# Kernel tuning notes

Hardware: AMD Instinct MI355X
Metric: run time of the kernel (lower is better)

Reference implementation:

```python
import jax, jax.numpy as jnp
import numpy as np

B, H, L, N = 128, 1024, 256, 64  # batch, d_model, seq len (l_max), SSM state size


def setup_inputs() -> dict:
    key = jax.random.key(0)
    ks = jax.random.split(key, 8)
    x = jax.random.normal(ks[0], (B, H, L), dtype=jnp.float32)
    # S4D init: dt log-uniform in [1e-3, 1e-1], A = -1/2 + i*pi*n, C ~ N(0,1)
    log_dt = jnp.log(10.0 ** jax.random.uniform(ks[1], (H,), minval=-3.0, maxval=-1.0)).astype(jnp.float32)
    A_real_log = jnp.log(0.5 * jnp.ones((H, N), dtype=jnp.float32))
    A_imag = jnp.tile(jnp.pi * jnp.arange(N, dtype=jnp.float32), (H, 1))
    C_re = jax.random.normal(ks[2], (H, N), dtype=jnp.float32)
    C_im = jax.random.normal(ks[3], (H, N), dtype=jnp.float32)
    D = jax.random.normal(ks[4], (H,), dtype=jnp.float32)
    W_out = (jax.random.normal(ks[5], (2 * H, H), dtype=jnp.float32) / np.sqrt(H)).astype(jnp.float32)
    b_out = jnp.zeros((2 * H,), dtype=jnp.float32)
    return dict(x=x, log_dt=log_dt, A_real_log=A_real_log, A_imag=A_imag,
                C_re=C_re, C_im=C_im, D=D, W_out=W_out, b_out=b_out)


def _s4d_kernel(log_dt, A_real_log, A_imag, C_re, C_im, length):
    """S4D convolution kernel (ZOH discretization), shape (H, length)."""
    dt = jnp.exp(log_dt)[:, None]                      # (H, 1)
    A = -jnp.exp(A_real_log) + 1j * A_imag             # (H, N) complex
    C = C_re + 1j * C_im                               # (H, N)
    dtA = A * dt                                       # (H, N)
    C_disc = C * (jnp.exp(dtA) - 1.0) / A              # ZOH-discretized C
    t = jnp.arange(length, dtype=jnp.float32)
    K = jnp.exp(dtA[:, :, None] * t)                   # (H, N, L) Vandermonde
    return 2.0 * jnp.einsum('hn,hnl->hl', C_disc, K).real


def reference(x, log_dt, A_real_log, A_imag, C_re, C_im, D, W_out, b_out):
    Bq, Hq, Lq = x.shape
    k = _s4d_kernel(log_dt, A_real_log, A_imag, C_re, C_im, Lq)  # (H, L)
    n_fft = 2 * Lq
    k_f = jnp.fft.rfft(k, n=n_fft)                     # (H, L+1)
    x_f = jnp.fft.rfft(x, n=n_fft, axis=-1)            # (B, H, L+1)
    y = jnp.fft.irfft(x_f * k_f[None], n=n_fft, axis=-1)[..., :Lq]
    y = y + D[None, :, None] * x                       # skip connection
    y = jax.nn.gelu(y)                                 # FFTConv activation
    # output linear (d_model -> 2*d_model) + GLU over channel dim
    y = jnp.einsum('bhl,gh->bgl', y, W_out) + b_out[None, :, None]
    a, b = jnp.split(y, 2, axis=1)
    return a * jax.nn.sigmoid(b)                       # (B, H, L)
```

## Files before the change

kernel.cpp:

```cpp
#include <hip/hip_runtime.h>
#include <hip/hip_bf16.h>
#include <cstdint>
#include <cstddef>

typedef __bf16 bf16x8 __attribute__((ext_vector_type(8)));
typedef float  f32x4  __attribute__((ext_vector_type(4)));
typedef unsigned short u16x8 __attribute__((ext_vector_type(8)));

__device__ __forceinline__ unsigned short f2bf(float f) {
    unsigned u = __builtin_bit_cast(unsigned, f);
    u += 0x7fffu + ((u >> 16) & 1u);
    return (unsigned short)(u >> 16);
}
__device__ __forceinline__ float bf2f(unsigned short u) {
    unsigned v = ((unsigned)u) << 16;
    return __builtin_bit_cast(float, v);
}
__device__ __forceinline__ float gelu_tanh(float x) {
    float z = 0.7978845608028654f * (x + 0.044715f * x * x * x);
    float e = __expf(2.0f * z);
    float t = 1.0f - 2.0f / (e + 1.0f);
    return 0.5f * x * (1.0f + t);
}

__global__ void k_build(const float* __restrict__ log_dt,
                        const float* __restrict__ arl,
                        const float* __restrict__ aim,
                        const float* __restrict__ cre,
                        const float* __restrict__ cim,
                        const float* __restrict__ Dp,
                        unsigned short* __restrict__ Tg) {
    __shared__ float sRe[64], sIm[64], sCr[64], sCi[64];
    __shared__ float kk[256];
    const int h = blockIdx.x;
    const int t = threadIdx.x;
    if (t < 64) {
        float dt  = expf(log_dt[h]);
        float ar  = -expf(arl[h * 64 + t]);
        float ai  = aim[h * 64 + t];
        float dre = ar * dt, dim = ai * dt;
        float er  = expf(dre);
        float s, c;
        sincosf(dim, &s, &c);
        float em1r = er * c - 1.0f, em1i = er * s;
        float cr = cre[h * 64 + t], ci = cim[h * 64 + t];
        float pr = cr * em1r - ci * em1i;
        float pi = cr * em1i + ci * em1r;
        float inv = 1.0f / (ar * ar + ai * ai);
        sCr[t] = (pr * ar + pi * ai) * inv;
        sCi[t] = (pi * ar - pr * ai) * inv;
        sRe[t] = dre; sIm[t] = dim;
    }
    __syncthreads();
    float acc = 0.0f;
    const float tf = (float)t;
    #pragma unroll 8
    for (int n = 0; n < 64; n++) {
        float er = expf(sRe[n] * tf);
        float s, c;
        sincosf(sIm[n] * tf, &s, &c);
        acc += sCr[n] * er * c - sCi[n] * er * s;
    }
    kk[t] = 2.0f * acc;
    __syncthreads();
    const float Dh = Dp[h];
    unsigned short* dst = Tg + (size_t)h * 16384;
    for (int c = t; c < 1024; c += 256) {
        const int d = c >> 6, q4 = (c >> 4) & 3, mm = c & 15;
        u16x8 hv, lv;
        #pragma unroll
        for (int e = 0; e < 8; e++) {
            const int idx = 16 * d + mm - (q4 * 8 + e);
            float v = (idx >= 0) ? kk[idx] : 0.0f;
            if (idx == 0) v += Dh;
            unsigned short hb = f2bf(v);
            hv[e] = hb;
            lv[e] = f2bf(v - bf2f(hb));
        }
        *(u16x8*)(dst + c * 8)        = hv;
        *(u16x8*)(dst + 8192 + c * 8) = lv;
    }
}

__global__ __launch_bounds__(256, 2)
void conv_mfma(const float* __restrict__ x,
               const unsigned short* __restrict__ Tg,
               unsigned short* __restrict__ yt2) {
    __shared__ __align__(16) unsigned short smem[32768];
    const int h = blockIdx.x, tid = threadIdx.x;
    const int w = tid >> 6, lane = tid & 63, m = lane & 15, q4 = lane >> 4;

    {
        const unsigned short* tg = Tg + (size_t)h * 16384;
        #pragma unroll
        for (int i = 0; i < 8; i++) {
            int q = i * 256 + tid;
            __builtin_amdgcn_global_load_lds(
                (const __attribute__((address_space(1))) void*)(tg + q * 8),
                (__attribute__((address_space(3))) void*)(smem + q * 8), 16, 0, 0);
        }
    }

    const int sb = tid >> 1;
    const float* xrow = x + (((size_t)(sb * 1024 + h)) << 8) + (tid & 1) * 16;

    {
        float4 v0 = *(const float4*)(xrow + 0);
        float4 v1 = *(const float4*)(xrow + 4);
        float4 v2 = *(const float4*)(xrow + 8);
        float4 v3 = *(const float4*)(xrow + 12);
        unsigned short* Xn = smem + 16384;
        const int qb = (tid & 1) * 2;
        #pragma unroll
        for (int s = 0; s < 4; s++) {
            float4 v = (s == 0) ? v0 : (s == 1) ? v1 : (s == 2) ? v2 : v3;
            const int q = qb + (s >> 1), off = (s & 1) * 4;
            ushort4 hv, lv;
            hv.x = f2bf(v.x); lv.x = f2bf(v.x - bf2f(hv.x));
            hv.y = f2bf(v.y); lv.y = f2bf(v.y - bf2f(hv.y));
            hv.z = f2bf(v.z); lv.z = f2bf(v.z - bf2f(hv.z));
            hv.w = f2bf(v.w); lv.w = f2bf(v.w - bf2f(hv.w));
            *(ushort4*)(Xn + (q * 128 + sb) * 8 + off)        = hv;
            *(ushort4*)(Xn + 4096 + (q * 128 + sb) * 8 + off) = lv;
        }
    }

    f32x4 acc[8][4];
    #pragma unroll
    for (int a = 0; a < 8; a++)
        #pragma unroll
        for (int b = 0; b < 4; b++) acc[a][b] = (f32x4){0.f, 0.f, 0.f, 0.f};

    __syncthreads();

    const int fi = (q4 * 16 + m) * 8;

    #pragma unroll 1
    for (int jt = 0; jt < 8; jt++) {
        const unsigned short* Xb = smem + 16384 + (jt & 1) * 8192;
        float4 p0, p1, p2, p3;
        if (jt < 7) {
            const float* xp = xrow + (jt + 1) * 32;
            p0 = *(const float4*)(xp + 0);
            p1 = *(const float4*)(xp + 4);
            p2 = *(const float4*)(xp + 8);
            p3 = *(const float4*)(xp + 12);
        }
        const int j2 = jt << 1;
        const bool a0 = (w      >= j2);
        const bool a1 = (w + 4  >= j2);
        const bool a2 = (w + 8  >= j2);
        const bool a3 = (w + 12 >= j2);
        bf16x8 th0, tl0, th1, tl1, th2, tl2, th3, tl3;
        if (a0) { int d = w      - j2; th0 = *(const bf16x8*)(smem + d * 512 + fi); tl0 = *(const bf16x8*)(smem + 8192 + d * 512 + fi); }
        if (a1) { int d = w + 4  - j2; th1 = *(const bf16x8*)(smem + d * 512 + fi); tl1 = *(const bf16x8*)(smem + 8192 + d * 512 + fi); }
        if (a2) { int d = w + 8  - j2; th2 = *(const bf16x8*)(smem + d * 512 + fi); tl2 = *(const bf16x8*)(smem + 8192 + d * 512 + fi); }
        if (a3) { int d = w + 12 - j2; th3 = *(const bf16x8*)(smem + d * 512 + fi); tl3 = *(const bf16x8*)(smem + 8192 + d * 512 + fi); }
        #pragma unroll
        for (int fb = 0; fb < 8; fb++) {
            const int xo = (q4 * 128 + fb * 16 + m) * 8;
            bf16x8 xh = *(const bf16x8*)(Xb + xo);
            bf16x8 xl = *(const bf16x8*)(Xb + 4096 + xo);
            if (a0) { acc[fb][0] = __builtin_amdgcn_mfma_f32_16x16x32_bf16(xh, th0, acc[fb][0], 0, 0, 0);
                      acc[fb][0] = __builtin_amdgcn_mfma_f32_16x16x32_bf16(xl, th0, acc[fb][0], 0, 0, 0);
                      acc[fb][0] = __builtin_amdgcn_mfma_f32_16x16x32_bf16(xh, tl0, acc[fb][0], 0, 0, 0); }
            if (a1) { acc[fb][1] = __builtin_amdgcn_mfma_f32_16x16x32_bf16(xh, th1, acc[fb][1], 0, 0, 0);
                      acc[fb][1] = __builtin_amdgcn_mfma_f32_16x16x32_bf16(xl, th1, acc[fb][1], 0, 0, 0);
                      acc[fb][1] = __builtin_amdgcn_mfma_f32_16x16x32_bf16(xh, tl1, acc[fb][1], 0, 0, 0); }
            if (a2) { acc[fb][2] = __builtin_amdgcn_mfma_f32_16x16x32_bf16(xh, th2, acc[fb][2], 0, 0, 0);
                      acc[fb][2] = __builtin_amdgcn_mfma_f32_16x16x32_bf16(xl, th2, acc[fb][2], 0, 0, 0);
                      acc[fb][2] = __builtin_amdgcn_mfma_f32_16x16x32_bf16(xh, tl2, acc[fb][2], 0, 0, 0); }
            if (a3) { acc[fb][3] = __builtin_amdgcn_mfma_f32_16x16x32_bf16(xh, th3, acc[fb][3], 0, 0, 0);
                      acc[fb][3] = __builtin_amdgcn_mfma_f32_16x16x32_bf16(xl, th3, acc[fb][3], 0, 0, 0);
                      acc[fb][3] = __builtin_amdgcn_mfma_f32_16x16x32_bf16(xh, tl3, acc[fb][3], 0, 0, 0); }
        }
        if (jt < 7) {
            unsigned short* Xn = smem + 16384 + ((jt + 1) & 1) * 8192;
            const int qb = (tid & 1) * 2;
            #pragma unroll
            for (int s = 0; s < 4; s++) {
                float4 v = (s == 0) ? p0 : (s == 1) ? p1 : (s == 2) ? p2 : p3;
                const int q = qb + (s >> 1), off = (s & 1) * 4;
                ushort4 hv, lv;
                hv.x = f2bf(v.x); lv.x = f2bf(v.x - bf2f(hv.x));
                hv.y = f2bf(v.y); lv.y = f2bf(v.y - bf2f(hv.y));
                hv.z = f2bf(v.z); lv.z = f2bf(v.z - bf2f(hv.z));
                hv.w = f2bf(v.w); lv.w = f2bf(v.w - bf2f(hv.w));
                *(ushort4*)(Xn + (q * 128 + sb) * 8 + off)        = hv;
                *(ushort4*)(Xn + 4096 + (q * 128 + sb) * 8 + off) = lv;
            }
        }
        __syncthreads();
    }

    const size_t ybase = (size_t)h * 32768;
    #pragma unroll
    for (int p = 0; p < 2; p++) {
        #pragma unroll
        for (int tt = 0; tt < 2; tt++) {
            const int ti = p * 2 + tt;
            const int lr = (w + 4 * ti) * 16 + m - p * 128;
            #pragma unroll
            for (int fb = 0; fb < 8; fb++) {
                #pragma unroll
                for (int rg = 0; rg < 4; rg++) {
                    const int b = fb * 16 + q4 * 4 + rg;
                    smem[b * 136 + lr] = f2bf(gelu_tanh(acc[fb][ti][rg]));
                }
            }
        }
        __syncthreads();
        #pragma unroll
        for (int bb = 0; bb < 4; bb++) {
            const int bp = bb * 32 + (tid >> 3);
            #pragma unroll
            for (int s = 0; s < 2; s++) {
                const int chk = (tid & 7) + 8 * s;
                u16x8 v = *(const u16x8*)(smem + bp * 136 + chk * 8);
                *(u16x8*)(yt2 + ybase + (size_t)bp * 256 + p * 128 + chk * 8) = v;
            }
        }
        __syncthreads();
    }
}

__global__ void transp(const unsigned short* __restrict__ yt2,
                       unsigned short* __restrict__ yt) {
    __shared__ __align__(16) unsigned short tl[4096];
    const int tid = threadIdx.x;
    const int m0 = blockIdx.x * 64, h0 = blockIdx.y * 64;
    {
        const int r0 = tid >> 3, ch = tid & 7;
        #pragma unroll
        for (int rr = 0; rr < 64; rr += 32) {
            const int r = r0 + rr;
            u16x8 v = *(const u16x8*)(yt2 + (size_t)(h0 + r) * 32768 + m0 + ch * 8);
            const int pch = ch ^ (r & 7) ^ ((r >> 3) & 7);
            *(u16x8*)(tl + r * 64 + pch * 8) = v;
        }
    }
    __syncthreads();
    {
        const int hc = tid & 7;
        #pragma unroll
        for (int mmr = 0; mmr < 64; mmr += 32) {
            const int mm = (tid >> 3) + mmr;
            u16x8 o;
            #pragma unroll
            for (int e = 0; e < 8; e++) {
                const int hh = hc * 8 + e;
                const int pm = (((mm >> 3) ^ (hh & 7) ^ ((hh >> 3) & 7)) << 3) + (mm & 7);
                o[e] = tl[hh * 64 + pm];
            }
            *(u16x8*)(yt + (size_t)(m0 + mm) * 1024 + h0 + hc * 8) = o;
        }
    }
}

__global__ void pack_w2(const float* __restrict__ W, unsigned short* __restrict__ Wp) {
    const int p   = blockIdx.x;
    const int g32 = p >> 5, r32 = p & 31;
    const int g   = (r32 < 16) ? (g32 * 16 + r32) : (1024 + g32 * 16 + (r32 - 16));
    const int t   = threadIdx.x;
    const float4 v = *(const float4*)(W + (size_t)g * 1024 + t * 4);
    ushort4 o;
    o.x = f2bf(v.x); o.y = f2bf(v.y); o.z = f2bf(v.z); o.w = f2bf(v.w);
    *(ushort4*)(Wp + (size_t)p * 1024 + t * 4) = o;
}

__global__ __launch_bounds__(512, 2)
void gemm_glu2(const unsigned short* __restrict__ yt,
               const unsigned short* __restrict__ Wp,
               const float* __restrict__ bo,
               float* __restrict__ out) {
    __shared__ __align__(16) unsigned short smem[65536];
    const int tid = threadIdx.x;
    const int bid = (int)blockIdx.x;
    const int b1  = (bid & 7) * 128 + (bid >> 3);
    const int bm  = b1 >> 3;
    const int bn  = b1 & 3 | (b1 & 7);
    const int bn_ = b1 & 7;
    const int wid = tid >> 6, lane = tid & 63;
    const int m = lane & 15, q4 = lane >> 4;
    const int wm = wid >> 2, wn = wid & 3;

    const size_t abase = (size_t)bm * 256 * 1024;
    const size_t bbase = (size_t)bn_ * 256 * 1024;

    f32x4 acc[8][4];
    #pragma unroll
    for (int fr = 0; fr < 8; fr++)
        #pragma unroll
        for (int fc = 0; fc < 4; fc++) acc[fr][fc] = (f32x4){0.f, 0.f, 0.f, 0.f};

    auto STAGE = [&](int t) {
        const int bufo = (t & 1) << 15;
        const int k0 = t * 64;
        #pragma unroll
        for (int i = 0; i < 4; i++) {
            int q = i * 512 + tid;
            int r = q >> 3, c = (q & 7) ^ (r & 7);
            const unsigned short* gp = yt + abase + (size_t)r * 1024 + k0 + c * 8;
            __builtin_amdgcn_global_load_lds(
                (const __attribute__((address_space(1))) void*)gp,
                (__attribute__((address_space(3))) void*)(smem + bufo + q * 8), 16, 0, 0);
        }
        #pragma unroll
        for (int i = 0; i < 4; i++) {
            int q = i * 512 + tid;
            int r = q >> 3, c = (q & 7) ^ (r & 7);
            const unsigned short* gp = Wp + bbase + (size_t)r * 1024 + k0 + c * 8;
            __builtin_amdgcn_global_load_lds(
                (const __attribute__((address_space(1))) void*)gp,
                (__attribute__((address_space(3))) void*)(smem + bufo + 16384 + q * 8), 16, 0, 0);
        }
    };

    STAGE(0);
    STAGE(1);
    asm volatile("s_waitcnt vmcnt(8)" ::: "memory");
    __builtin_amdgcn_s_barrier();

    const int arow0 = wm * 128;
    const int brow0 = wn * 64;

    for (int t = 0; t < 16; t++) {
        const int bufo = (t & 1) << 15;
        bf16x8 af[8][2], bf[4][2];
        #pragma unroll
        for (int fr = 0; fr < 8; fr++) {
            const int r = arow0 + fr * 16 + m;
            #pragma unroll
            for (int ks = 0; ks < 2; ks++) {
                const int c = (ks * 4 + q4) ^ (r & 7);
                af[fr][ks] = *(const bf16x8*)(smem + bufo + r * 64 + c * 8);
            }
        }
        #pragma unroll
        for (int fc = 0; fc < 4; fc++) {
            const int r = brow0 + fc * 16 + m;
            #pragma unroll
            for (int ks = 0; ks < 2; ks++) {
                const int c = (ks * 4 + q4) ^ (r & 7);
                bf[fc][ks] = *(const bf16x8*)(smem + bufo + 16384 + r * 64 + c * 8);
            }
        }
        asm volatile("s_waitcnt lgkmcnt(0)" ::: "memory");
        __builtin_amdgcn_sched_barrier(0);
        __builtin_amdgcn_s_barrier();
        if (t < 14) STAGE(t + 2);
        __builtin_amdgcn_s_setprio(1);
        #pragma unroll
        for (int ks = 0; ks < 2; ks++)
            #pragma unroll
            for (int fr = 0; fr < 8; fr++)
                #pragma unroll
                for (int fc = 0; fc < 4; fc++)
                    acc[fr][fc] = __builtin_amdgcn_mfma_f32_16x16x32_bf16(
                        af[fr][ks], bf[fc][ks], acc[fr][fc], 0, 0, 0);
        __builtin_amdgcn_s_setprio(0);
        if (t < 14) asm volatile("s_waitcnt vmcnt(8)" ::: "memory");
        else        asm volatile("s_waitcnt vmcnt(0)" ::: "memory");
        __builtin_amdgcn_s_barrier();
    }

    const size_t outb = ((size_t)bm) << 18;
    const int lbase = wm * 128;
    #pragma unroll
    for (int fcp = 0; fcp < 2; fcp++) {
        const int go = (bn_ * 8 + wn * 2 + fcp) * 16 + m;
        const float boa = bo[go], bog = bo[1024 + go];
        #pragma unroll
        for (int fr = 0; fr < 8; fr++) {
            f32x4 av = acc[fr][2 * fcp];
            f32x4 gv = acc[fr][2 * fcp + 1];
            f32x4 o;
            #pragma unroll
            for (int rg = 0; rg < 4; rg++) {
                float a = av[rg] + boa, g = gv[rg] + bog;
                o[rg] = a / (1.0f + __expf(-g));
            }
            const int l = lbase + fr * 16 + q4 * 4;
            *(f32x4*)(out + outb + (((size_t)go) << 8) + l) = o;
        }
    }
    (void)bn;
}

extern "C" void kernel_launch(void* const* d_in, const int* in_sizes, int n_in,
                              void* d_out, int out_size, void* d_ws, size_t ws_size,
                              hipStream_t stream) {
    const float* x   = (const float*)d_in[0];
    const float* ldt = (const float*)d_in[1];
    const float* arl = (const float*)d_in[2];
    const float* aim = (const float*)d_in[3];
    const float* cre = (const float*)d_in[4];
    const float* cim = (const float*)d_in[5];
    const float* D   = (const float*)d_in[6];
    const float* Wo  = (const float*)d_in[7];
    const float* bo  = (const float*)d_in[8];
    float* out = (float*)d_out;

    const size_t MB = (size_t)1 << 20;
    const size_t need = 132 * MB;
    if (ws_size < need) return;

    unsigned short* Wp  = (unsigned short*)d_ws;
    unsigned short* Tg  = (unsigned short*)((char*)d_ws + 4 * MB);
    unsigned short* yt  = (unsigned short*)((char*)d_ws + 4 * MB);
    unsigned short* yt2 = (unsigned short*)((char*)d_ws + 68 * MB);

    k_build  <<<1024, 256, 0, stream>>>(ldt, arl, aim, cre, cim, D, Tg);
    pack_w2  <<<2048, 256, 0, stream>>>(Wo, Wp);
    conv_mfma<<<1024, 256, 0, stream>>>(x, Tg, yt2);
    transp   <<<dim3(512, 16), 256, 0, stream>>>(yt2, yt);
    gemm_glu2<<<1024, 512, 0, stream>>>(yt, Wp, bo, out);
}
```

Baseline: 441.4 us.

## Enlarge transpose tiles, split GLU GEMM into two N-half launches, use sincospi

The transpose kernel now moves 128x256 tiles per block instead of 64x64, with a padded, XOR-swizzled shared buffer, so fewer blocks each do more work. The output GEMM is split into two launches that each cover half of the N tiles, with a new block-to-tile mapping, apparently to improve L2 reuse of the weight and activation tiles. The S4D kernel build uses sincospif on a pre-scaled argument instead of sincosf. Risks include lower occupancy from the 66KB transpose tile and the cost of an extra launch.

```diff
diff --git a/kernel.cpp b/kernel.cpp
--- a/kernel.cpp
+++ b/kernel.cpp
@@ -30,7 +30,7 @@
                         const float* __restrict__ cim,
                         const float* __restrict__ Dp,
                         unsigned short* __restrict__ Tg) {
-    __shared__ float sRe[64], sIm[64], sCr[64], sCi[64];
+    __shared__ float sRe[64], sW[64], sCr[64], sCi[64];
     __shared__ float kk[256];
     const int h = blockIdx.x;
     const int t = threadIdx.x;
@@ -49,7 +49,8 @@
         float inv = 1.0f / (ar * ar + ai * ai);
         sCr[t] = (pr * ar + pi * ai) * inv;
         sCi[t] = (pi * ar - pr * ai) * inv;
-        sRe[t] = dre; sIm[t] = dim;
+        sRe[t] = dre;
+        sW[t]  = dim * 0.31830988618379067f;
     }
     __syncthreads();
     float acc = 0.0f;
@@ -58,7 +59,7 @@
     for (int n = 0; n < 64; n++) {
         float er = expf(sRe[n] * tf);
         float s, c;
-        sincosf(sIm[n] * tf, &s, &c);
+        sincospif(sW[n] * tf, &s, &c);
         acc += sCr[n] * er * c - sCi[n] * er * s;
     }
     kk[t] = 2.0f * acc;
@@ -226,34 +227,28 @@
 
 __global__ void transp(const unsigned short* __restrict__ yt2,
                        unsigned short* __restrict__ yt) {
-    __shared__ __align__(16) unsigned short tl[4096];
+    __shared__ __align__(16) unsigned short tl[128 * 264];
     const int tid = threadIdx.x;
-    const int m0 = blockIdx.x * 64, h0 = blockIdx.y * 64;
-    {
-        const int r0 = tid >> 3, ch = tid & 7;
-        #pragma unroll
-        for (int rr = 0; rr < 64; rr += 32) {
-            const int r = r0 + rr;
-            u16x8 v = *(const u16x8*)(yt2 + (size_t)(h0 + r) * 32768 + m0 + ch * 8);
-            const int pch = ch ^ (r & 7) ^ ((r >> 3) & 7);
-            *(u16x8*)(tl + r * 64 + pch * 8) = v;
-        }
+    const int m0 = blockIdx.x * 256, h0 = blockIdx.y * 128;
+    #pragma unroll
+    for (int i = 0; i < 16; i++) {
+        const int q = i * 256 + tid;
+        const int hh = q >> 5, c = q & 31;
+        u16x8 v = *(const u16x8*)(yt2 + (size_t)(h0 + hh) * 32768 + m0 + c * 8);
+        *(u16x8*)(tl + hh * 264 + ((c ^ (hh & 31)) << 3)) = v;
     }
     __syncthreads();
-    {
-        const int hc = tid & 7;
-        #pragma unroll
-        for (int mmr = 0; mmr < 64; mmr += 32) {
-            const int mm = (tid >> 3) + mmr;
-            u16x8 o;
-            #pragma unroll
-            for (int e = 0; e < 8; e++) {
-                const int hh = hc * 8 + e;
-                const int pm = (((mm >> 3) ^ (hh & 7) ^ ((hh >> 3) & 7)) << 3) + (mm & 7);
-                o[e] = tl[hh * 64 + pm];
-            }
-            *(u16x8*)(yt + (size_t)(m0 + mm) * 1024 + h0 + hc * 8) = o;
-        }
+    #pragma unroll
+    for (int i = 0; i < 16; i++) {
+        const int q = i * 256 + tid;
+        const int mm = q >> 4, hc = q & 15;
+        u16x8 o;
+        #pragma unroll
+        for (int e = 0; e < 8; e++) {
+            const int hh = hc * 8 + e;
+            o[e] = tl[hh * 264 + (((mm >> 3) ^ (hh & 31)) << 3) + (mm & 7)];
+        }
+        *(u16x8*)(yt + (size_t)(m0 + mm) * 1024 + h0 + hc * 8) = o;
     }
 }
 
@@ -272,14 +267,14 @@
 void gemm_glu2(const unsigned short* __restrict__ yt,
                const unsigned short* __restrict__ Wp,
                const float* __restrict__ bo,
-               float* __restrict__ out) {
+               float* __restrict__ out,
+               int bn_off) {
     __shared__ __align__(16) unsigned short smem[65536];
     const int tid = threadIdx.x;
     const int bid = (int)blockIdx.x;
-    const int b1  = (bid & 7) * 128 + (bid >> 3);
-    const int bm  = b1 >> 3;
-    const int bn  = b1 & 3 | (b1 & 7);
-    const int bn_ = b1 & 7;
+    const int b1  = (bid & 7) * 64 + (bid >> 3);
+    const int bm  = b1 >> 2;
+    const int bn_ = bn_off + (b1 & 3);
     const int wid = tid >> 6, lane = tid & 63;
     const int m = lane & 15, q4 = lane >> 4;
     const int wm = wid >> 2, wn = wid & 3;
@@ -384,7 +379,6 @@
             *(f32x4*)(out + outb + (((size_t)go) << 8) + l) = o;
         }
     }
-    (void)bn;
 }
 
 extern "C" void kernel_launch(void* const* d_in, const int* in_sizes, int n_in,
@@ -413,6 +407,7 @@
     k_build  <<<1024, 256, 0, stream>>>(ldt, arl, aim, cre, cim, D, Tg);
     pack_w2  <<<2048, 256, 0, stream>>>(Wo, Wp);
     conv_mfma<<<1024, 256, 0, stream>>>(x, Tg, yt2);
-    transp   <<<dim3(512, 16), 256, 0, stream>>>(yt2, yt);
-    gemm_glu2<<<1024, 512, 0, stream>>>(yt, Wp, bo, out);
-}
+    transp   <<<dim3(128, 8), 256, 0, stream>>>(yt2, yt);
+    gemm_glu2<<<512, 512, 0, stream>>>(yt, Wp, bo, out, 0);
+    gemm_glu2<<<512, 512, 0, stream>>>(yt, Wp, bo, out, 4);
+}
```

After: 458.5 us. 3.9% more time.
